# Performance work log

Hardware: AMD Instinct MI355X
Metric: run time of the kernel (lower is better)

## Reference

```python
import jax, jax.numpy as jnp
import numpy as np

B, C, H, W = 4, 32, 128, 256
EPS = 1e-5  # BatchNorm eps


def _conv1x1_bn(x, w, b, gamma, beta, mean, var):
    # x: [B,C,H,W]; 1x1 conv == channel matmul, fused with eval-mode BatchNorm
    y = jnp.einsum('bchw,oc->bohw', x, w) + b[None, :, None, None]
    scale = gamma / jnp.sqrt(var + EPS)
    shift = beta - mean * scale
    return y * scale[None, :, None, None] + shift[None, :, None, None]


def setup_inputs() -> dict:
    key = jax.random.key(0)
    ks = jax.random.split(key, 15)
    d = {
        'x_left': jax.random.normal(ks[0], (B, C, H, W), jnp.float32),
        'x_right': jax.random.normal(ks[1], (B, C, H, W), jnp.float32),
        'cost': jax.random.normal(ks[2], (2, B, H, W, W), jnp.float32),
        'q_w': jax.random.normal(ks[3], (C, C), jnp.float32),
        'q_b': jax.random.normal(ks[4], (C,), jnp.float32),
        'q_gamma': jax.random.uniform(ks[5], (C,), jnp.float32),
        'q_beta': jax.random.normal(ks[6], (C,), jnp.float32),
        'q_mean': jax.random.normal(ks[7], (C,), jnp.float32),
        'q_var': jax.random.uniform(ks[8], (C,), jnp.float32),
        'k_w': jax.random.normal(ks[9], (C, C), jnp.float32),
        'k_b': jax.random.normal(ks[10], (C,), jnp.float32),
        'k_gamma': jax.random.uniform(ks[11], (C,), jnp.float32),
        'k_beta': jax.random.normal(ks[12], (C,), jnp.float32),
        'k_mean': jax.random.normal(ks[13], (C,), jnp.float32),
        'k_var': jax.random.uniform(ks[14], (C,), jnp.float32),
    }
    return d


def reference(x_left, x_right, cost, q_w, q_b, q_gamma, q_beta, q_mean, q_var,
              k_w, k_b, k_gamma, k_beta, k_mean, k_var):
    b, c, h, w = x_left.shape
    cr = w // 3  # clamped_range

    # band masks: right2left keeps 0 <= i-j < cr (lower band); left2right keeps 0 <= j-i < cr
    idx = jnp.arange(w)
    diff = idx[:, None] - idx[None, :]  # [W,W] = i - j
    low_band = ((diff >= 0) & (diff < cr)).astype(x_left.dtype)
    up_band = low_band.T

    # right-to-left: Q from left, K from right
    q_l = jnp.transpose(_conv1x1_bn(x_left, q_w, q_b, q_gamma, q_beta, q_mean, q_var), (0, 2, 3, 1))   # [B,H,W,C]
    k_r = jnp.transpose(_conv1x1_bn(x_right, k_w, k_b, k_gamma, k_beta, k_mean, k_var), (0, 2, 3, 1))  # [B,H,W,C]
    s_r2l = jnp.einsum('bhic,bhjc->bhij', q_l, k_r) / c  # [B,H,W,W]
    cost_r2l = s_r2l * low_band + cost[0]

    # left-to-right: Q from right, K from left
    q_r = jnp.transpose(_conv1x1_bn(x_right, q_w, q_b, q_gamma, q_beta, q_mean, q_var), (0, 2, 3, 1))
    k_l = jnp.transpose(_conv1x1_bn(x_left, k_w, k_b, k_gamma, k_beta, k_mean, k_var), (0, 2, 3, 1))
    s_l2r = jnp.einsum('bhic,bhjc->bhij', q_r, k_l) / c
    cost_l2r = s_l2r * up_band + cost[1]

    # original returns (x_left + fea_left, x_right + fea_right, (r2l, l2r)) with fea == x
    return (x_left * 2.0, x_right * 2.0, cost_r2l, cost_l2r)
```

## Files before the change

kernel.cpp:

```cpp
#include <hip/hip_runtime.h>

#define BB 4
#define CC 32
#define HH 128
#define WW 256
#define CR 85
#define EPSF 1e-5f

#define O1_OFF 4194304
#define O2_OFF 8388608
#define COST1 33554432

typedef __attribute__((ext_vector_type(8))) short bf16x8;
typedef __attribute__((ext_vector_type(4))) float f32x4;
typedef __attribute__((ext_vector_type(4))) float f4v;

#define ARR (512 * 256 * 32)
#define WS_Q(side) ((side) * ARR)
#define WS_K(side) (2 * ARR + (side) * ARR)
#define WS_NEEDED (4ull * ARR * 2ull)

static __device__ __forceinline__ unsigned short f2bf(float f) {
    unsigned u = __float_as_uint(f);
    unsigned r = (u + 0x7FFFu + ((u >> 16) & 1u)) >> 16;
    return (unsigned short)r;
}

__global__ __launch_bounds__(256, 4)
void proj_kernel(const float* __restrict__ x_left, const float* __restrict__ x_right,
                 const float* __restrict__ q_w, const float* __restrict__ q_b,
                 const float* __restrict__ q_gamma, const float* __restrict__ q_beta,
                 const float* __restrict__ q_mean, const float* __restrict__ q_var,
                 const float* __restrict__ k_w, const float* __restrict__ k_b,
                 const float* __restrict__ k_gamma, const float* __restrict__ k_beta,
                 const float* __restrict__ k_mean, const float* __restrict__ k_var,
                 float* __restrict__ out, unsigned short* __restrict__ ws)
{
    __shared__ float wq[CC][CC];
    __shared__ float wk[CC][CC];
    __shared__ float bq[CC], bk[CC], sq[CC], sk[CC];

    const int t    = threadIdx.x;
    const int side = blockIdx.x >> 9;
    const int bh   = blockIdx.x & 511;

    if (t < CC) {
        float qs = q_gamma[t] * rsqrtf(q_var[t] + EPSF);
        float ks = k_gamma[t] * rsqrtf(k_var[t] + EPSF);
        sq[t] = qs; sk[t] = ks;
        bq[t] = q_b[t] * qs + q_beta[t] - q_mean[t] * qs;
        bk[t] = k_b[t] * ks + k_beta[t] - k_mean[t] * ks;
    }
    __syncthreads();
    for (int r = t; r < CC * CC; r += 256) {
        int o = r >> 5, c = r & 31;
        wq[c][o] = q_w[r] * sq[o];
        wk[c][o] = k_w[r] * sk[o];
    }
    __syncthreads();

    float q[CC], k[CC];
    #pragma unroll
    for (int o = 0; o < CC; ++o) { q[o] = bq[o]; k[o] = bk[o]; }

    const float* x = side ? x_right : x_left;
    const int b = bh >> 7, h = bh & 127;
    const int xbase = (b * CC * HH + h) * WW + t;
    float* outx = out + side * O1_OFF;

    #pragma unroll 4
    for (int c = 0; c < CC; ++c) {
        int idx = xbase + c * (HH * WW);
        float xv = __builtin_nontemporal_load(x + idx);
        __builtin_nontemporal_store(2.0f * xv, outx + idx);
        #pragma unroll
        for (int o = 0; o < CC; ++o) {
            q[o] += xv * wq[c][o];
            k[o] += xv * wk[c][o];
        }
    }

    unsigned short* qdst = ws + WS_Q(side) + (bh * WW + t) * CC;
    unsigned short* kdst = ws + WS_K(side) + (bh * WW + t) * CC;
    #pragma unroll
    for (int g = 0; g < 4; ++g) {
        uint4 vq, vk;
        vq.x = f2bf(q[8*g+0]) | ((unsigned)f2bf(q[8*g+1]) << 16);
        vq.y = f2bf(q[8*g+2]) | ((unsigned)f2bf(q[8*g+3]) << 16);
        vq.z = f2bf(q[8*g+4]) | ((unsigned)f2bf(q[8*g+5]) << 16);
        vq.w = f2bf(q[8*g+6]) | ((unsigned)f2bf(q[8*g+7]) << 16);
        vk.x = f2bf(k[8*g+0]) | ((unsigned)f2bf(k[8*g+1]) << 16);
        vk.y = f2bf(k[8*g+2]) | ((unsigned)f2bf(k[8*g+3]) << 16);
        vk.z = f2bf(k[8*g+4]) | ((unsigned)f2bf(k[8*g+5]) << 16);
        vk.w = f2bf(k[8*g+6]) | ((unsigned)f2bf(k[8*g+7]) << 16);
        ((uint4*)qdst)[g] = vq;
        ((uint4*)kdst)[g] = vk;
    }
}

__global__ __launch_bounds__(256, 5)
void score_kernel(const float* __restrict__ cost, const unsigned short* __restrict__ ws,
                  float* __restrict__ out)
{
    __shared__ char lds[32 * 132 * 4];
    unsigned short* Qs = (unsigned short*)lds;
    unsigned short* Ks = (unsigned short*)(lds + 2048);
    float* Sb = (float*)lds;

    const int t    = threadIdx.x;
    const int bx   = blockIdx.x;
    const int tile = bx & 7;
    const int bh   = (bx >> 3) & 511;
    const int dir  = bx >> 12;
    const int i0   = tile * 32;
    const int wbase = dir ? i0 : (i0 - 96);

    const float* csrc = cost + (size_t)dir * COST1 + (size_t)bh * (WW * WW);
    float* odst = out + O2_OFF + (size_t)dir * COST1 + (size_t)bh * (WW * WW);
    const int rowlane = t >> 6;
    const int c4 = 4 * (t & 63);

    f4v vbuf[8];
    #pragma unroll
    for (int p = 0; p < 8; ++p) {
        int rl = 4 * p + rowlane;
        vbuf[p] = __builtin_nontemporal_load((const f4v*)(csrc + (i0 + rl) * WW + c4));
    }

    const unsigned short* qsrc = ws + (dir ? WS_Q(1) : WS_Q(0)) + bh * WW * CC;
    const unsigned short* ksrc = ws + (dir ? WS_K(0) : WS_K(1)) + bh * WW * CC;

    if (t < 128) {
        ((uint4*)Qs)[t] = ((const uint4*)(qsrc + i0 * CC))[t];
    }
    {
        uint4* dst = (uint4*)Ks;
        #pragma unroll
        for (int qq = t; qq < 512; qq += 256) {
            int col = wbase + (qq >> 2);
            uint4 v = make_uint4(0u, 0u, 0u, 0u);
            if (col >= 0 && col < WW)
                v = ((const uint4*)(ksrc + col * CC))[qq & 3];
            dst[qq] = v;
        }
    }
    __syncthreads();

    const int w = t >> 6, lane = t & 63;
    const int quad = lane >> 4, l16 = lane & 15;
    f32x4 acc[2][2] = {};
    bf16x8 afrag[2], bfrag[2];
    #pragma unroll
    for (int mt = 0; mt < 2; ++mt)
        afrag[mt] = *(const bf16x8*)(Qs + (16 * mt + l16) * CC + quad * 8);
    #pragma unroll
    for (int nt = 0; nt < 2; ++nt)
        bfrag[nt] = *(const bf16x8*)(Ks + (32 * w + 16 * nt + l16) * CC + quad * 8);
    #pragma unroll
    for (int mt = 0; mt < 2; ++mt)
        #pragma unroll
        for (int nt = 0; nt < 2; ++nt)
            acc[mt][nt] = __builtin_amdgcn_mfma_f32_16x16x32_bf16(
                afrag[mt], bfrag[nt], acc[mt][nt], 0, 0, 0);
    __syncthreads();

    #pragma unroll
    for (int mt = 0; mt < 2; ++mt)
        #pragma unroll
        for (int nt = 0; nt < 2; ++nt) {
            int cl = 32 * w + 16 * nt + l16;
            #pragma unroll
            for (int r = 0; r < 4; ++r) {
                int row = 16 * mt + quad * 4 + r;
                Sb[row * 132 + cl] = acc[mt][nt][r];
            }
        }
    __syncthreads();

    const float inv32 = 1.0f / 32.0f;
    const int lc = c4 - wbase;
    const bool inwin = (lc >= 0 && lc < 128);

    #pragma unroll
    for (int p = 0; p < 8; ++p) {
        int rl = 4 * p + rowlane;
        int i = i0 + rl;
        f4v v = vbuf[p];
        if (inwin) {
            const f4v s = *(const f4v*)(Sb + rl * 132 + lc);
            int d0 = dir ? (c4 + 0 - i) : (i - c4 - 0);
            int d1 = dir ? (c4 + 1 - i) : (i - c4 - 1);
            int d2 = dir ? (c4 + 2 - i) : (i - c4 - 2);
            int d3 = dir ? (c4 + 3 - i) : (i - c4 - 3);
            if (d0 >= 0 && d0 < CR) v[0] += s[0] * inv32;
            if (d1 >= 0 && d1 < CR) v[1] += s[1] * inv32;
            if (d2 >= 0 && d2 < CR) v[2] += s[2] * inv32;
            if (d3 >= 0 && d3 < CR) v[3] += s[3] * inv32;
        }
        __builtin_nontemporal_store(v, (f4v*)(odst + (size_t)i * WW + c4));
    }
}

__global__ __launch_bounds__(256, 2)
void pab_fused(const float* __restrict__ x_left, const float* __restrict__ x_right,
               const float* __restrict__ cost,
               const float* __restrict__ q_w, const float* __restrict__ q_b,
               const float* __restrict__ q_gamma, const float* __restrict__ q_beta,
               const float* __restrict__ q_mean, const float* __restrict__ q_var,
               const float* __restrict__ k_w, const float* __restrict__ k_b,
               const float* __restrict__ k_gamma, const float* __restrict__ k_beta,
               const float* __restrict__ k_mean, const float* __restrict__ k_var,
               float* __restrict__ out)
{
    __shared__ float qwt[CC][CC];
    __shared__ float kwt[CC][CC];
    __shared__ float qbf[CC], kbf[CC], qsc[CC], ksc[CC];
    __shared__ float Qls[WW][CC];
    __shared__ float Qrs[WW][CC];

    const int t   = threadIdx.x;
    const int bid = blockIdx.x;
    const int b   = bid >> 7;
    const int h   = bid & 127;

    if (t < CC) {
        float qs = q_gamma[t] * rsqrtf(q_var[t] + EPSF);
        float ks = k_gamma[t] * rsqrtf(k_var[t] + EPSF);
        qsc[t] = qs; ksc[t] = ks;
        qbf[t] = q_b[t] * qs + q_beta[t] - q_mean[t] * qs;
        kbf[t] = k_b[t] * ks + k_beta[t] - k_mean[t] * ks;
    }
    __syncthreads();
    for (int r = t; r < CC * CC; r += 256) {
        int o = r >> 5, c = r & 31;
        qwt[c][o] = q_w[r] * qsc[o];
        kwt[c][o] = k_w[r] * ksc[o];
    }
    __syncthreads();

    float ql[CC], qr[CC], kl[CC], kr[CC];
    #pragma unroll
    for (int o = 0; o < CC; ++o) {
        float qb0 = qbf[o], kb0 = kbf[o];
        ql[o] = qb0; qr[o] = qb0; kl[o] = kb0; kr[o] = kb0;
    }
    const int xbase = (b * CC * HH + h) * WW + t;
    #pragma unroll 4
    for (int c = 0; c < CC; ++c) {
        int idx = xbase + c * (HH * WW);
        float xl = x_left[idx];
        float xr = x_right[idx];
        out[idx]          = 2.0f * xl;
        out[O1_OFF + idx] = 2.0f * xr;
        #pragma unroll
        for (int o = 0; o < CC; ++o) {
            float qw = qwt[c][o];
            float kw = kwt[c][o];
            ql[o] += xl * qw;
            kl[o] += xl * kw;
            qr[o] += xr * qw;
            kr[o] += xr * kw;
        }
    }
    #pragma unroll
    for (int o = 0; o < CC; o += 4) {
        *(float4*)&Qls[t][o] = make_float4(ql[o], ql[o+1], ql[o+2], ql[o+3]);
        *(float4*)&Qrs[t][o] = make_float4(qr[o], qr[o+1], qr[o+2], qr[o+3]);
    }
    __syncthreads();

    const int rowbase = bid * (WW * WW) + t;
    const float* __restrict__ c0 = cost + rowbase;
    const float* __restrict__ c1 = cost + COST1 + rowbase;
    float* __restrict__ o2 = out + O2_OFF + rowbase;
    float* __restrict__ o3 = out + O2_OFF + COST1 + rowbase;

    #pragma unroll 2
    for (int i = 0; i < WW; ++i) {
        float v0 = c0[i * WW];
        float v1 = c1[i * WW];
        int d = i - t;
        if (d >= 0 && d < CR) {
            float s = 0.f;
            #pragma unroll
            for (int o = 0; o < CC; o += 4) {
                float4 q = *(const float4*)&Qls[i][o];
                s += q.x * kr[o] + q.y * kr[o+1] + q.z * kr[o+2] + q.w * kr[o+3];
            }
            v0 += s * (1.0f / 32.0f);
        }
        if (d <= 0 && d > -CR) {
            float s = 0.f;
            #pragma unroll
            for (int o = 0; o < CC; o += 4) {
                float4 q = *(const float4*)&Qrs[i][o];
                s += q.x * kl[o] + q.y * kl[o+1] + q.z * kl[o+2] + q.w * kl[o+3];
            }
            v1 += s * (1.0f / 32.0f);
        }
        o2[i * WW] = v0;
        o3[i * WW] = v1;
    }
}

extern "C" void kernel_launch(void* const* d_in, const int* in_sizes, int n_in,
                              void* d_out, int out_size, void* d_ws, size_t ws_size,
                              hipStream_t stream) {
    const float* x_left  = (const float*)d_in[0];
    const float* x_right = (const float*)d_in[1];
    const float* cost    = (const float*)d_in[2];
    const float* q_w     = (const float*)d_in[3];
    const float* q_b     = (const float*)d_in[4];
    const float* q_gamma = (const float*)d_in[5];
    const float* q_beta  = (const float*)d_in[6];
    const float* q_mean  = (const float*)d_in[7];
    const float* q_var   = (const float*)d_in[8];
    const float* k_w     = (const float*)d_in[9];
    const float* k_b     = (const float*)d_in[10];
    const float* k_gamma = (const float*)d_in[11];
    const float* k_beta  = (const float*)d_in[12];
    const float* k_mean  = (const float*)d_in[13];
    const float* k_var   = (const float*)d_in[14];
    float* out = (float*)d_out;

    if (ws_size >= WS_NEEDED) {
        unsigned short* ws = (unsigned short*)d_ws;
        proj_kernel<<<dim3(1024), dim3(256), 0, stream>>>(
            x_left, x_right,
            q_w, q_b, q_gamma, q_beta, q_mean, q_var,
            k_w, k_b, k_gamma, k_beta, k_mean, k_var,
            out, ws);
        score_kernel<<<dim3(8192), dim3(256), 0, stream>>>(cost, ws, out);
    } else {
        pab_fused<<<dim3(BB * HH), dim3(256), 0, stream>>>(
            x_left, x_right, cost,
            q_w, q_b, q_gamma, q_beta, q_mean, q_var,
            k_w, k_b, k_gamma, k_beta, k_mean, k_var,
            out);
    }
}
```

Baseline: 543.4 us.

## Apply band scores directly from MFMA registers and drop LDS score staging

The score kernel now computes the transposed product (K×Q) so each lane's MFMA accumulator lines up with contiguous output columns. Each wave loads the matching cost fragment, adds the masked scores in registers and stores it directly, so the LDS staging buffer and its two barriers are gone. Cost columns outside the score window are copied separately with a new 32-column-block thread mapping. The stores become 16-byte per-lane fragments spread across rows rather than fully coalesced rows, which may hurt memory efficiency.

```diff
diff --git a/kernel.cpp b/kernel.cpp
--- a/kernel.cpp
+++ b/kernel.cpp
@@ -102,10 +102,8 @@
 void score_kernel(const float* __restrict__ cost, const unsigned short* __restrict__ ws,
                   float* __restrict__ out)
 {
-    __shared__ char lds[32 * 132 * 4];
-    unsigned short* Qs = (unsigned short*)lds;
-    unsigned short* Ks = (unsigned short*)(lds + 2048);
-    float* Sb = (float*)lds;
+    __shared__ unsigned short Qs[32 * CC];
+    __shared__ unsigned short Ks[128 * CC];
 
     const int t    = threadIdx.x;
     const int bx   = blockIdx.x;
@@ -114,90 +112,92 @@
     const int dir  = bx >> 12;
     const int i0   = tile * 32;
     const int wbase = dir ? i0 : (i0 - 96);
-
-    const float* csrc = cost + (size_t)dir * COST1 + (size_t)bh * (WW * WW);
-    float* odst = out + O2_OFF + (size_t)dir * COST1 + (size_t)bh * (WW * WW);
-    const int rowlane = t >> 6;
-    const int c4 = 4 * (t & 63);
-
-    f4v vbuf[8];
-    #pragma unroll
-    for (int p = 0; p < 8; ++p) {
-        int rl = 4 * p + rowlane;
-        vbuf[p] = __builtin_nontemporal_load((const f4v*)(csrc + (i0 + rl) * WW + c4));
-    }
+    const int wp0   = wbase >> 5;
 
     const unsigned short* qsrc = ws + (dir ? WS_Q(1) : WS_Q(0)) + bh * WW * CC;
     const unsigned short* ksrc = ws + (dir ? WS_K(0) : WS_K(1)) + bh * WW * CC;
+    const float* csrc = cost + (size_t)dir * COST1 + (size_t)bh * (WW * WW) + (size_t)i0 * WW;
+    float* odst = out + O2_OFF + (size_t)dir * COST1 + (size_t)bh * (WW * WW) + (size_t)i0 * WW;
 
     if (t < 128) {
         ((uint4*)Qs)[t] = ((const uint4*)(qsrc + i0 * CC))[t];
     }
-    {
-        uint4* dst = (uint4*)Ks;
-        #pragma unroll
-        for (int qq = t; qq < 512; qq += 256) {
-            int col = wbase + (qq >> 2);
-            uint4 v = make_uint4(0u, 0u, 0u, 0u);
-            if (col >= 0 && col < WW)
-                v = ((const uint4*)(ksrc + col * CC))[qq & 3];
-            dst[qq] = v;
-        }
+    #pragma unroll
+    for (int qq = t; qq < 512; qq += 256) {
+        int col = wbase + (qq >> 2);
+        uint4 v = make_uint4(0u, 0u, 0u, 0u);
+        if (col >= 0 && col < WW)
+            v = ((const uint4*)(ksrc + col * CC))[qq & 3];
+        ((uint4*)Ks)[qq] = v;
     }
     __syncthreads();
 
     const int w = t >> 6, lane = t & 63;
     const int quad = lane >> 4, l16 = lane & 15;
+    const int pw = wp0 + w;
+    const bool wvalid = (pw >= 0 && pw < 8);
+
+    const int prow = t >> 3;
+    const int pc4  = 4 * (t & 7);
+    f4v cbuf[8];
+    #pragma unroll
+    for (int p = 0; p < 8; ++p) {
+        if (p < wp0 || p > wp0 + 3)
+            cbuf[p] = __builtin_nontemporal_load((const f4v*)(csrc + prow * WW + p * 32 + pc4));
+    }
+
+    f4v wv[2][2];
+    if (wvalid) {
+        #pragma unroll
+        for (int nt = 0; nt < 2; ++nt)
+            #pragma unroll
+            for (int mt = 0; mt < 2; ++mt) {
+                int i  = 16 * mt + l16;
+                int jb = 32 * pw + 16 * nt + 4 * quad;
+                wv[nt][mt] = __builtin_nontemporal_load((const f4v*)(csrc + i * WW + jb));
+            }
+    }
+
+    bf16x8 kf[2], qf[2];
+    #pragma unroll
+    for (int nt = 0; nt < 2; ++nt)
+        kf[nt] = *(const bf16x8*)(Ks + (32 * w + 16 * nt + l16) * CC + quad * 8);
+    #pragma unroll
+    for (int mt = 0; mt < 2; ++mt)
+        qf[mt] = *(const bf16x8*)(Qs + (16 * mt + l16) * CC + quad * 8);
+
     f32x4 acc[2][2] = {};
-    bf16x8 afrag[2], bfrag[2];
-    #pragma unroll
-    for (int mt = 0; mt < 2; ++mt)
-        afrag[mt] = *(const bf16x8*)(Qs + (16 * mt + l16) * CC + quad * 8);
     #pragma unroll
     for (int nt = 0; nt < 2; ++nt)
-        bfrag[nt] = *(const bf16x8*)(Ks + (32 * w + 16 * nt + l16) * CC + quad * 8);
-    #pragma unroll
-    for (int mt = 0; mt < 2; ++mt)
+        #pragma unroll
+        for (int mt = 0; mt < 2; ++mt)
+            acc[nt][mt] = __builtin_amdgcn_mfma_f32_16x16x32_bf16(
+                kf[nt], qf[mt], acc[nt][mt], 0, 0, 0);
+
+    if (wvalid) {
+        const float inv32 = 1.0f / 32.0f;
         #pragma unroll
         for (int nt = 0; nt < 2; ++nt)
-            acc[mt][nt] = __builtin_amdgcn_mfma_f32_16x16x32_bf16(
-                afrag[mt], bfrag[nt], acc[mt][nt], 0, 0, 0);
-    __syncthreads();
-
-    #pragma unroll
-    for (int mt = 0; mt < 2; ++mt)
-        #pragma unroll
-        for (int nt = 0; nt < 2; ++nt) {
-            int cl = 32 * w + 16 * nt + l16;
             #pragma unroll
-            for (int r = 0; r < 4; ++r) {
-                int row = 16 * mt + quad * 4 + r;
-                Sb[row * 132 + cl] = acc[mt][nt][r];
+            for (int mt = 0; mt < 2; ++mt) {
+                int i  = 16 * mt + l16;
+                int ia = i0 + i;
+                int jb = 32 * pw + 16 * nt + 4 * quad;
+                f4v v = wv[nt][mt];
+                #pragma unroll
+                for (int r = 0; r < 4; ++r) {
+                    int j = jb + r;
+                    int d = dir ? (j - ia) : (ia - j);
+                    if (d >= 0 && d < CR) v[r] += acc[nt][mt][r] * inv32;
+                }
+                __builtin_nontemporal_store(v, (f4v*)(odst + i * WW + jb));
             }
-        }
-    __syncthreads();
-
-    const float inv32 = 1.0f / 32.0f;
-    const int lc = c4 - wbase;
-    const bool inwin = (lc >= 0 && lc < 128);
+    }
 
     #pragma unroll
     for (int p = 0; p < 8; ++p) {
-        int rl = 4 * p + rowlane;
-        int i = i0 + rl;
-        f4v v = vbuf[p];
-        if (inwin) {
-            const f4v s = *(const f4v*)(Sb + rl * 132 + lc);
-            int d0 = dir ? (c4 + 0 - i) : (i - c4 - 0);
-            int d1 = dir ? (c4 + 1 - i) : (i - c4 - 1);
-            int d2 = dir ? (c4 + 2 - i) : (i - c4 - 2);
-            int d3 = dir ? (c4 + 3 - i) : (i - c4 - 3);
-            if (d0 >= 0 && d0 < CR) v[0] += s[0] * inv32;
-            if (d1 >= 0 && d1 < CR) v[1] += s[1] * inv32;
-            if (d2 >= 0 && d2 < CR) v[2] += s[2] * inv32;
-            if (d3 >= 0 && d3 < CR) v[3] += s[3] * inv32;
-        }
-        __builtin_nontemporal_store(v, (f4v*)(odst + (size_t)i * WW + c4));
+        if (p < wp0 || p > wp0 + 3)
+            __builtin_nontemporal_store(cbuf[p], (f4v*)(odst + prow * WW + p * 32 + pc4));
     }
 }
 
```

Measured after the change: 562.5 us. 1.04x slower.

## Load MFMA fragments directly from global and remap block order

Applied to the files above, without the earlier changes.

Drops staging of Q and K tiles through shared memory. Each wave now loads its bf16 MFMA fragments straight from global memory, which removes two barriers and the LDS round trip. Block indices are also permuted so that consecutive blocks sweep (b,h) rows with a fixed tile, changing the order of cost and workspace accesses. The trade-off is some redundant global loads of Q and K across waves, and possible locality changes from the remap.

```diff
diff --git a/kernel.cpp b/kernel.cpp
--- a/kernel.cpp
+++ b/kernel.cpp
@@ -102,21 +102,21 @@
 void score_kernel(const float* __restrict__ cost, const unsigned short* __restrict__ ws,
                   float* __restrict__ out)
 {
-    __shared__ char lds[32 * 132 * 4];
-    unsigned short* Qs = (unsigned short*)lds;
-    unsigned short* Ks = (unsigned short*)(lds + 2048);
-    float* Sb = (float*)lds;
-
-    const int t    = threadIdx.x;
-    const int bx   = blockIdx.x;
+    __shared__ float Sb[32 * 132];
+
+    const int bx   = (blockIdx.x & 7) * 1024 + (blockIdx.x >> 3);
     const int tile = bx & 7;
     const int bh   = (bx >> 3) & 511;
     const int dir  = bx >> 12;
     const int i0   = tile * 32;
     const int wbase = dir ? i0 : (i0 - 96);
 
+    const unsigned short* qsrc = ws + (dir ? WS_Q(1) : WS_Q(0)) + bh * WW * CC;
+    const unsigned short* ksrc = ws + (dir ? WS_K(0) : WS_K(1)) + bh * WW * CC;
     const float* csrc = cost + (size_t)dir * COST1 + (size_t)bh * (WW * WW);
     float* odst = out + O2_OFF + (size_t)dir * COST1 + (size_t)bh * (WW * WW);
+
+    const int t = threadIdx.x;
     const int rowlane = t >> 6;
     const int c4 = 4 * (t & 63);
 
@@ -127,42 +127,29 @@
         vbuf[p] = __builtin_nontemporal_load((const f4v*)(csrc + (i0 + rl) * WW + c4));
     }
 
-    const unsigned short* qsrc = ws + (dir ? WS_Q(1) : WS_Q(0)) + bh * WW * CC;
-    const unsigned short* ksrc = ws + (dir ? WS_K(0) : WS_K(1)) + bh * WW * CC;
-
-    if (t < 128) {
-        ((uint4*)Qs)[t] = ((const uint4*)(qsrc + i0 * CC))[t];
-    }
-    {
-        uint4* dst = (uint4*)Ks;
-        #pragma unroll
-        for (int qq = t; qq < 512; qq += 256) {
-            int col = wbase + (qq >> 2);
-            uint4 v = make_uint4(0u, 0u, 0u, 0u);
-            if (col >= 0 && col < WW)
-                v = ((const uint4*)(ksrc + col * CC))[qq & 3];
-            dst[qq] = v;
-        }
-    }
-    __syncthreads();
-
     const int w = t >> 6, lane = t & 63;
     const int quad = lane >> 4, l16 = lane & 15;
+
+    bf16x8 qf[2], kf[2];
+    #pragma unroll
+    for (int mt = 0; mt < 2; ++mt)
+        qf[mt] = *(const bf16x8*)(qsrc + (i0 + 16 * mt + l16) * CC + quad * 8);
+    #pragma unroll
+    for (int nt = 0; nt < 2; ++nt) {
+        int col = wbase + 32 * w + 16 * nt + l16;
+        bf16x8 kv = {};
+        if (col >= 0 && col < WW)
+            kv = *(const bf16x8*)(ksrc + col * CC + quad * 8);
+        kf[nt] = kv;
+    }
+
     f32x4 acc[2][2] = {};
-    bf16x8 afrag[2], bfrag[2];
-    #pragma unroll
-    for (int mt = 0; mt < 2; ++mt)
-        afrag[mt] = *(const bf16x8*)(Qs + (16 * mt + l16) * CC + quad * 8);
-    #pragma unroll
-    for (int nt = 0; nt < 2; ++nt)
-        bfrag[nt] = *(const bf16x8*)(Ks + (32 * w + 16 * nt + l16) * CC + quad * 8);
     #pragma unroll
     for (int mt = 0; mt < 2; ++mt)
         #pragma unroll
         for (int nt = 0; nt < 2; ++nt)
             acc[mt][nt] = __builtin_amdgcn_mfma_f32_16x16x32_bf16(
-                afrag[mt], bfrag[nt], acc[mt][nt], 0, 0, 0);
-    __syncthreads();
+                qf[mt], kf[nt], acc[mt][nt], 0, 0, 0);
 
     #pragma unroll
     for (int mt = 0; mt < 2; ++mt)
```

Measured after the change: 547.3 us. Within noise of the previous version (+0.7%).
